# Performance work log

Measured on AMD Instinct MI355X. Metric: run time of the kernel, lower is better.

Reference implementation:

```python
import jax, jax.numpy as jnp
import numpy as np

N_AGENT, N_TRACK, D_IN, HEADS, OUT, E = 50000, 200000, 128, 4, 64, 500000
NEG_SLOPE = 0.2  # PyG GATConv default negative_slope


def segment_softmax(scores, seg, n):
    # PyG softmax: subtract per-segment max, exp, divide by per-segment sum (+1e-16)
    m = jax.ops.segment_max(scores, seg, num_segments=n)
    m = jnp.where(jnp.isneginf(m), 0.0, m)  # guard empty segments
    e = jnp.exp(scores - m[seg])
    s = jax.ops.segment_sum(e, seg, num_segments=n)
    return e / (s[seg] + 1e-16)


def gat_conv(x_src, x_dst, e_src, e_dst, W, a_src, a_dst, b):
    # PyG GATConv, concat=False, add_self_loops=False, eval mode (no dropout)
    H, C = a_src.shape
    n_dst = x_dst.shape[0]
    xs = (x_src @ W).reshape(-1, H, C)   # [Ns,H,C]
    xd = (x_dst @ W).reshape(-1, H, C)   # [Nd,H,C] (same lin for src and dst)
    al_s = jnp.einsum('nhc,hc->nh', xs, a_src)
    al_d = jnp.einsum('nhc,hc->nh', xd, a_dst)
    alpha = jax.nn.leaky_relu(al_s[e_src] + al_d[e_dst], NEG_SLOPE)  # [E,H]
    alpha = segment_softmax(alpha, e_dst, n_dst)
    msg = xs[e_src] * alpha[:, :, None]                               # [E,H,C]
    out = jax.ops.segment_sum(msg, e_dst, num_segments=n_dst)         # [Nd,H,C]
    return out.mean(axis=1) + b  # concat=False -> mean over heads, then bias


def setup_inputs() -> dict:
    key = jax.random.key(0)
    ks = jax.random.split(key, 16)
    inp = {
        'x_agent': jax.random.normal(ks[0], (N_AGENT, D_IN), jnp.float32),
        'x_track': jax.random.normal(ks[1], (N_TRACK, D_IN), jnp.float32),
        'W': jax.random.normal(ks[2], (4, D_IN, HEADS * OUT), jnp.float32) * 0.1,
        'att_src': jax.random.normal(ks[3], (4, HEADS, OUT), jnp.float32) * 0.1,
        'att_dst': jax.random.normal(ks[4], (4, HEADS, OUT), jnp.float32) * 0.1,
        'bias': jax.random.normal(ks[5], (4, OUT), jnp.float32) * 0.1,
    }
    # relations 0,2: agent->track ; relations 1,3: track->agent
    srcs = [N_AGENT, N_TRACK, N_AGENT, N_TRACK]
    dsts = [N_TRACK, N_AGENT, N_TRACK, N_AGENT]
    for r in range(4):
        inp[f'e{r}_src'] = jax.random.randint(ks[6 + 2 * r], (E,), 0, srcs[r], jnp.int32)
        inp[f'e{r}_dst'] = jax.random.randint(ks[7 + 2 * r], (E,), 0, dsts[r], jnp.int32)
    return inp


def reference(x_agent, x_track, W, att_src, att_dst, bias,
              e0_src, e0_dst, e1_src, e1_dst, e2_src, e2_dst, e3_src, e3_dst):
    t0 = gat_conv(x_agent, x_track, e0_src, e0_dst, W[0], att_src[0], att_dst[0], bias[0])
    a1 = gat_conv(x_track, x_agent, e1_src, e1_dst, W[1], att_src[1], att_dst[1], bias[1])
    t2 = gat_conv(x_agent, x_track, e2_src, e2_dst, W[2], att_src[2], att_dst[2], bias[2])
    a3 = gat_conv(x_track, x_agent, e3_src, e3_dst, W[3], att_src[3], att_dst[3], bias[3])
    # HeteroConv aggr='mean' over relations sharing a dst node type
    out_agent = (a1 + a3) * 0.5
    out_track = (t0 + t2) * 0.5
    return out_agent, out_track
```

## Files before the change

### kernel.cpp

```cpp
#include <hip/hip_runtime.h>
#include <hip/hip_bf16.h>

typedef __attribute__((ext_vector_type(8))) short short8;
typedef __attribute__((ext_vector_type(4))) short short4v;
typedef __attribute__((ext_vector_type(4))) float f32x4;

__device__ __forceinline__ unsigned short f2bf(float f) {
  unsigned u = __builtin_bit_cast(unsigned, f);
  u += 0x7FFFu + ((u >> 16) & 1u);
  return (unsigned short)(u >> 16);
}
__device__ __forceinline__ float bf2f(unsigned short b) {
  unsigned u = ((unsigned)b) << 16;
  return __builtin_bit_cast(float, u);
}

__global__ void prep_u(const float* __restrict__ W, const float* __restrict__ att_src,
                       const float* __restrict__ att_dst,
                       float* __restrict__ U_agent, float* __restrict__ U_track) {
  int idx = blockIdx.x * 256 + threadIdx.x;
  if (idx >= 2 * 16 * 128) return;
  int which = idx >> 11;
  int rem = idx & 2047;
  int j = rem >> 7;
  int k = rem & 127;
  int r = j >> 2, h = j & 3;
  bool srcSide = (which == 0) ? ((r & 1) == 0) : ((r & 1) == 1);
  const float* att = (srcSide ? att_src : att_dst) + (r * 4 + h) * 64;
  const float* Wr = W + (r * 128 + k) * 256 + h * 64;
  float s = 0.f;
#pragma unroll 8
  for (int c = 0; c < 64; ++c) s += Wr[c] * att[c];
  (which ? U_track : U_agent)[j * 128 + k] = s;
}

__global__ void prep_wt(const float* __restrict__ W, unsigned short* __restrict__ Wt) {
  int idx = blockIdx.x * 256 + threadIdx.x;
  if (idx >= 4 * 256 * 128) return;
  int r = idx >> 15;
  int rem = idx & 32767;
  int c = rem >> 7;
  int k = rem & 127;
  Wt[idx] = f2bf(W[(r * 128 + k) * 256 + c]);
}

__global__ __launch_bounds__(256) void node_al2(const float* __restrict__ x,
                                                const float* __restrict__ U, int N,
                                                float* __restrict__ d0, float* __restrict__ d1,
                                                float* __restrict__ d2, float* __restrict__ d3) {
  __shared__ float xs[32 * 132];
  __shared__ float us[16 * 132];
  int tid = threadIdx.x;
  for (int i = tid; i < 2048; i += 256) us[(i >> 7) * 132 + (i & 127)] = U[i];
  int n0 = blockIdx.x * 32;
#pragma unroll
  for (int it = 0; it < 4; ++it) {
    int idx = (it * 256 + tid) * 4;
    int row = idx >> 7, k = idx & 127;
    float4 v = make_float4(0.f, 0.f, 0.f, 0.f);
    if (n0 + row < N) v = *(const float4*)(x + (size_t)(n0 + row) * 128 + k);
    *(float4*)&xs[row * 132 + k] = v;
  }
  __syncthreads();
  int node = tid >> 3;
  int g = n0 + node;
  if (g >= N) return;
  int j0 = (tid & 7) * 2;
  const float* xr = &xs[node * 132];
  const float* u0 = &us[j0 * 132];
  const float* u1 = &us[(j0 + 1) * 132];
  float a0 = 0.f, a1 = 0.f;
#pragma unroll
  for (int k = 0; k < 128; k += 4) {
    float4 xv = *(const float4*)(xr + k);
    float4 v0 = *(const float4*)(u0 + k);
    float4 v1 = *(const float4*)(u1 + k);
    a0 += xv.x * v0.x + xv.y * v0.y + xv.z * v0.z + xv.w * v0.w;
    a1 += xv.x * v1.x + xv.y * v1.y + xv.z * v1.z + xv.w * v1.w;
  }
  int r = j0 >> 2, h = j0 & 3;
  float* dp = (r == 0) ? d0 : (r == 1) ? d1 : (r == 2) ? d2 : d3;
  dp[(size_t)g * 4 + h] = a0;
  dp[(size_t)g * 4 + h + 1] = a1;
}

__global__ void init_out(float* __restrict__ out, const float* __restrict__ bias,
                         int NA, int NT) {
  int idx = blockIdx.x * 256 + threadIdx.x;
  int total4 = (NA + NT) * 16;
  if (idx >= total4) return;
  int f = idx * 4;
  int c = f & 63;
  const float *b0, *b1;
  if (f < NA * 64) { b0 = bias + 64; b1 = bias + 192; }
  else             { b0 = bias;      b1 = bias + 128; }
  float4 v;
  v.x = 0.5f * (b0[c] + b1[c]);
  v.y = 0.5f * (b0[c + 1] + b1[c + 1]);
  v.z = 0.5f * (b0[c + 2] + b1[c + 2]);
  v.w = 0.5f * (b0[c + 3] + b1[c + 3]);
  *(float4*)(out + f) = v;
}

__global__ __launch_bounds__(256) void proj_gemm(const float* __restrict__ X,
                                                 const unsigned short* __restrict__ Wt,
                                                 unsigned short* __restrict__ P, int Ns) {
  __shared__ unsigned short Xs[64 * 136];
  __shared__ unsigned short Ws[128 * 136];
  int tid = threadIdx.x;
  int m0 = blockIdx.x * 64;
  int cs = blockIdx.y * 128;
#pragma unroll
  for (int it = 0; it < 8; ++it) {
    int idx = (tid + it * 256) * 4;
    int row = idx >> 7, k = idx & 127;
    int g = m0 + row;
    float4 v = make_float4(0.f, 0.f, 0.f, 0.f);
    if (g < Ns) v = *(const float4*)(X + (size_t)g * 128 + k);
    short4v sv;
    sv.x = (short)f2bf(v.x); sv.y = (short)f2bf(v.y);
    sv.z = (short)f2bf(v.z); sv.w = (short)f2bf(v.w);
    *(short4v*)&Xs[row * 136 + k] = sv;
  }
#pragma unroll
  for (int it = 0; it < 8; ++it) {
    int idx = (tid + it * 256) * 8;
    int row = idx >> 7, k = idx & 127;
    short8 v = *(const short8*)(Wt + (size_t)(cs + row) * 128 + k);
    *(short8*)&Ws[row * 136 + k] = v;
  }
  __syncthreads();
  int lane = tid & 63, w = tid >> 6;
  f32x4 acc[8];
#pragma unroll
  for (int t = 0; t < 8; ++t) acc[t] = (f32x4){0.f, 0.f, 0.f, 0.f};
  int aoff = (w * 16 + (lane & 15)) * 136 + (lane >> 4) * 8;
  int boff = (lane & 15) * 136 + (lane >> 4) * 8;
#pragma unroll
  for (int kc = 0; kc < 4; ++kc) {
    short8 a = *(const short8*)&Xs[aoff + kc * 32];
#pragma unroll
    for (int t = 0; t < 8; ++t) {
      short8 b = *(const short8*)&Ws[boff + t * 16 * 136 + kc * 32];
      acc[t] = __builtin_amdgcn_mfma_f32_16x16x32_bf16(a, b, acc[t], 0, 0, 0);
    }
  }
#pragma unroll
  for (int t = 0; t < 8; ++t) {
#pragma unroll
    for (int q = 0; q < 4; ++q) {
      int grow = m0 + w * 16 + (lane >> 4) * 4 + q;
      if (grow < Ns) P[(size_t)grow * 256 + cs + t * 16 + (lane & 15)] = f2bf(acc[t][q]);
    }
  }
}

__global__ void csr_hist(const int* __restrict__ edst, int* __restrict__ count, int E) {
  int e = blockIdx.x * 256 + threadIdx.x;
  if (e < E) atomicAdd(&count[edst[e]], 1);
}

__global__ void csr_base(const int* __restrict__ count, int* __restrict__ cursor,
                         int* __restrict__ base, int* __restrict__ fill, int Nd) {
  int d = blockIdx.x * 256 + threadIdx.x;
  if (d >= Nd) return;
  int c = count[d];
  int b = atomicAdd(cursor, c);
  base[d] = b;
  fill[d] = b;
}

__global__ void csr_scatter(const int* __restrict__ esrc, const int* __restrict__ edst,
                            int* __restrict__ fill, int* __restrict__ elist, int E) {
  int e = blockIdx.x * 256 + threadIdx.x;
  if (e < E) {
    int pos = atomicAdd(&fill[edst[e]], 1);
    elist[pos] = esrc[e];
  }
}

__global__ __launch_bounds__(256) void passB_v3(
    const int* __restrict__ count, const int* __restrict__ base,
    const int* __restrict__ elist,
    const float* __restrict__ alS, const float* __restrict__ alD,
    const unsigned short* __restrict__ P, float* __restrict__ outp, int Nd) {
  int grp = (blockIdx.x * 256 + threadIdx.x) >> 5;
  if (grp >= Nd) return;
  int l = threadIdx.x & 31;
  int h = l >> 3;
  int cb = (l & 7) * 8;
  int cnt = count[grp];
  int b = base[grp];
  float ad = alD[(size_t)grp * 4 + h];
  int loff = h * 64 + cb;

  float den = 0.f;
  float acc[8];
#pragma unroll
  for (int j = 0; j < 8; ++j) acc[j] = 0.f;

  for (int i = 0; i < cnt; i += 2) {
    bool two = (i + 1 < cnt);
    int s0 = elist[b + i];
    int s1 = two ? elist[b + i + 1] : s0;
    float v0 = alS[(size_t)s0 * 4 + h] + ad;
    float v1 = alS[(size_t)s1 * 4 + h] + ad;
    short8 p0 = *(const short8*)(P + (size_t)s0 * 256 + loff);
    short8 p1 = *(const short8*)(P + (size_t)s1 * 256 + loff);
    v0 = v0 > 0.f ? v0 : 0.2f * v0;
    v1 = v1 > 0.f ? v1 : 0.2f * v1;
    float e0 = __expf(v0);
    float e1 = two ? __expf(v1) : 0.f;
    den += e0 + e1;
#pragma unroll
    for (int j = 0; j < 8; ++j)
      acc[j] += e0 * bf2f((unsigned short)p0[j]) + e1 * bf2f((unsigned short)p1[j]);
  }

  float q = 0.125f / (den + 1e-16f);
#pragma unroll
  for (int j = 0; j < 8; ++j) {
    float a = acc[j] * q;
    a += __shfl_xor(a, 8);
    a += __shfl_xor(a, 16);
    acc[j] = a;
  }
  if (l < 8) {
    float* op = outp + (size_t)grp * 64 + l * 8;
    float4 c0 = *(float4*)op;
    float4 c1 = *(float4*)(op + 4);
    c0.x += acc[0]; c0.y += acc[1]; c0.z += acc[2]; c0.w += acc[3];
    c1.x += acc[4]; c1.y += acc[5]; c1.z += acc[6]; c1.w += acc[7];
    *(float4*)op = c0;
    *(float4*)(op + 4) = c1;
  }
}

extern "C" void kernel_launch(void* const* d_in, const int* in_sizes, int n_in,
                              void* d_out, int out_size, void* d_ws, size_t ws_size,
                              hipStream_t stream) {
  const float* x_agent = (const float*)d_in[0];
  const float* x_track = (const float*)d_in[1];
  const float* W = (const float*)d_in[2];
  const float* att_src = (const float*)d_in[3];
  const float* att_dst = (const float*)d_in[4];
  const float* bias = (const float*)d_in[5];
  const int* es[4] = {(const int*)d_in[6], (const int*)d_in[8],
                      (const int*)d_in[10], (const int*)d_in[12]};
  const int* ed[4] = {(const int*)d_in[7], (const int*)d_in[9],
                      (const int*)d_in[11], (const int*)d_in[13]};
  int NA = in_sizes[0] / 128;
  int NT = in_sizes[1] / 128;
  float* out = (float*)d_out;

  int Ns[4] = {NA, NT, NA, NT};
  int Nd[4] = {NT, NA, NT, NA};
  const float* xsrc[4] = {x_agent, x_track, x_agent, x_track};

  char* ws = (char*)d_ws;
  size_t off = 0;
  auto alloc = [&](size_t bytes) -> void* {
    void* p = ws + off;
    off += (bytes + 255) & ~(size_t)255;
    return p;
  };
  int maxN = NA > NT ? NA : NT;
  int maxE = 0;
  for (int r = 0; r < 4; ++r) maxE = in_sizes[6 + 2 * r] > maxE ? in_sizes[6 + 2 * r] : maxE;

  unsigned short* P = (unsigned short*)alloc((size_t)maxN * 256 * 2);
  float *alS[4], *alD[4];
  for (int r = 0; r < 4; ++r) alS[r] = (float*)alloc((size_t)Ns[r] * 4 * 4);
  for (int r = 0; r < 4; ++r) alD[r] = (float*)alloc((size_t)Nd[r] * 4 * 4);
  float* U_agent = (float*)alloc(16 * 128 * 4);
  float* U_track = (float*)alloc(16 * 128 * 4);
  unsigned short* Wt = (unsigned short*)alloc(4 * 256 * 128 * 2);
  int* count = (int*)alloc(((size_t)maxN + 1) * 4);
  int* base = (int*)alloc((size_t)maxN * 4);
  int* fill = (int*)alloc((size_t)maxN * 4);
  int* elist = (int*)alloc((size_t)maxE * 4);

  prep_u<<<16, 256, 0, stream>>>(W, att_src, att_dst, U_agent, U_track);
  prep_wt<<<512, 256, 0, stream>>>(W, Wt);

  node_al2<<<(NA + 31) / 32, 256, 0, stream>>>(x_agent, U_agent, NA,
                                               alS[0], alD[1], alS[2], alD[3]);
  node_al2<<<(NT + 31) / 32, 256, 0, stream>>>(x_track, U_track, NT,
                                               alD[0], alS[1], alD[2], alS[3]);

  int total4 = (NA + NT) * 16;
  init_out<<<(total4 + 255) / 256, 256, 0, stream>>>(out, bias, NA, NT);

  for (int r = 0; r < 4; ++r) {
    int E = in_sizes[6 + 2 * r];
    int nd = Nd[r];
    int* cursor = count + maxN;
    hipMemsetAsync(count, 0, ((size_t)maxN + 1) * 4, stream);
    csr_hist<<<(E + 255) / 256, 256, 0, stream>>>(ed[r], count, E);
    csr_base<<<(nd + 255) / 256, 256, 0, stream>>>(count, cursor, base, fill, nd);
    csr_scatter<<<(E + 255) / 256, 256, 0, stream>>>(es[r], ed[r], fill, elist, E);

    dim3 pg((Ns[r] + 63) / 64, 2);
    proj_gemm<<<pg, 256, 0, stream>>>(xsrc[r], Wt + (size_t)r * 256 * 128, P, Ns[r]);

    float* outp = (r & 1) ? out : out + (size_t)NA * 64;
    passB_v3<<<(nd + 7) / 8, 256, 0, stream>>>(count, base, elist,
                                               alS[r], alD[r], P, outp, nd);
  }
}
```

Baseline: 971.5 us.

## Fuse agent-to-track relations into one CSR and aggregation pass, drop init_out

Relations 0 and 2 now share one CSR build, with both edge lists stored per destination and source indices offset into a stacked projection buffer. A single passB_track kernel then aggregates both relations per track node and writes the final output with the averaged bias. The separate init_out pass and the read-modify-write of the output are removed for the first write to each output region. This saves launches, one output init pass and one read-modify-write over the track output, at the cost of a larger P buffer and more code.

Measured after the change: 849.4 us. 12.6% less time.

```diff
diff --git a/kernel.cpp b/kernel.cpp
--- a/kernel.cpp
+++ b/kernel.cpp
@@ -34,6 +34,13 @@
   (which ? U_track : U_agent)[j * 128 + k] = s;
 }
 
+__global__ void prep_bias(const float* __restrict__ bias,
+                          float* __restrict__ bavgT, float* __restrict__ bavgA) {
+  int c = threadIdx.x;
+  if (c < 64) bavgT[c] = 0.5f * (bias[c] + bias[128 + c]);
+  else if (c < 128) bavgA[c - 64] = 0.5f * (bias[64 + c - 64] + bias[192 + c - 64]);
+}
+
 __global__ void prep_wt(const float* __restrict__ W, unsigned short* __restrict__ Wt) {
   int idx = blockIdx.x * 256 + threadIdx.x;
   if (idx >= 4 * 256 * 128) return;
@@ -82,24 +89,6 @@
   float* dp = (r == 0) ? d0 : (r == 1) ? d1 : (r == 2) ? d2 : d3;
   dp[(size_t)g * 4 + h] = a0;
   dp[(size_t)g * 4 + h + 1] = a1;
-}
-
-__global__ void init_out(float* __restrict__ out, const float* __restrict__ bias,
-                         int NA, int NT) {
-  int idx = blockIdx.x * 256 + threadIdx.x;
-  int total4 = (NA + NT) * 16;
-  if (idx >= total4) return;
-  int f = idx * 4;
-  int c = f & 63;
-  const float *b0, *b1;
-  if (f < NA * 64) { b0 = bias + 64; b1 = bias + 192; }
-  else             { b0 = bias;      b1 = bias + 128; }
-  float4 v;
-  v.x = 0.5f * (b0[c] + b1[c]);
-  v.y = 0.5f * (b0[c + 1] + b1[c + 1]);
-  v.z = 0.5f * (b0[c + 2] + b1[c + 2]);
-  v.w = 0.5f * (b0[c + 3] + b1[c + 3]);
-  *(float4*)(out + f) = v;
 }
 
 __global__ __launch_bounds__(256) void proj_gemm(const float* __restrict__ X,
@@ -160,45 +149,140 @@
   if (e < E) atomicAdd(&count[edst[e]], 1);
 }
 
-__global__ void csr_base(const int* __restrict__ count, int* __restrict__ cursor,
-                         int* __restrict__ base, int* __restrict__ fill, int Nd) {
+__global__ void csr_base2(const int* __restrict__ cntA, const int* __restrict__ cntB,
+                          int* __restrict__ cursor, int* __restrict__ base,
+                          int* __restrict__ fillA, int* __restrict__ fillB, int Nd) {
   int d = blockIdx.x * 256 + threadIdx.x;
   if (d >= Nd) return;
-  int c = count[d];
-  int b = atomicAdd(cursor, c);
+  int c0 = cntA[d], c2 = cntB[d];
+  int b = atomicAdd(cursor, c0 + c2);
   base[d] = b;
-  fill[d] = b;
+  fillA[d] = b;
+  fillB[d] = b + c0;
 }
 
 __global__ void csr_scatter(const int* __restrict__ esrc, const int* __restrict__ edst,
-                            int* __restrict__ fill, int* __restrict__ elist, int E) {
+                            int* __restrict__ fill, int* __restrict__ elist,
+                            int rowoff, int E) {
   int e = blockIdx.x * 256 + threadIdx.x;
   if (e < E) {
     int pos = atomicAdd(&fill[edst[e]], 1);
-    elist[pos] = esrc[e];
-  }
-}
-
-__global__ __launch_bounds__(256) void passB_v3(
-    const int* __restrict__ count, const int* __restrict__ base,
-    const int* __restrict__ elist,
-    const float* __restrict__ alS, const float* __restrict__ alD,
-    const unsigned short* __restrict__ P, float* __restrict__ outp, int Nd) {
+    elist[pos] = esrc[e] + rowoff;
+  }
+}
+
+__global__ __launch_bounds__(256) void passB_track(
+    const int* __restrict__ cntA, const int* __restrict__ cntB,
+    const int* __restrict__ base, const int* __restrict__ elist,
+    const float* __restrict__ alSA, const float* __restrict__ alD0,
+    const float* __restrict__ alD2, const unsigned short* __restrict__ P,
+    const float* __restrict__ bavg, float* __restrict__ outp, int Nd) {
   int grp = (blockIdx.x * 256 + threadIdx.x) >> 5;
   if (grp >= Nd) return;
   int l = threadIdx.x & 31;
   int h = l >> 3;
-  int cb = (l & 7) * 8;
+  int loff = h * 64 + (l & 7) * 8;
+  int c0 = cntA[grp], c2 = cntB[grp];
+  int b = base[grp];
+  float ad0 = alD0[(size_t)grp * 4 + h];
+  float ad2 = alD2[(size_t)grp * 4 + h];
+
+  float res[8];
+#pragma unroll
+  for (int j = 0; j < 8; ++j) res[j] = 0.f;
+  float acc[8];
+
+  {
+    float den = 0.f;
+#pragma unroll
+    for (int j = 0; j < 8; ++j) acc[j] = 0.f;
+    for (int i = 0; i < c0; i += 2) {
+      bool two = (i + 1 < c0);
+      int s0 = elist[b + i];
+      int s1 = two ? elist[b + i + 1] : s0;
+      float v0 = alSA[(size_t)s0 * 4 + h] + ad0;
+      float v1 = alSA[(size_t)s1 * 4 + h] + ad0;
+      short8 p0 = *(const short8*)(P + (size_t)s0 * 256 + loff);
+      short8 p1 = *(const short8*)(P + (size_t)s1 * 256 + loff);
+      v0 = v0 > 0.f ? v0 : 0.2f * v0;
+      v1 = v1 > 0.f ? v1 : 0.2f * v1;
+      float e0 = __expf(v0);
+      float e1 = two ? __expf(v1) : 0.f;
+      den += e0 + e1;
+#pragma unroll
+      for (int j = 0; j < 8; ++j)
+        acc[j] += e0 * bf2f((unsigned short)p0[j]) + e1 * bf2f((unsigned short)p1[j]);
+    }
+    float q = 0.125f / (den + 1e-16f);
+#pragma unroll
+    for (int j = 0; j < 8; ++j) res[j] += acc[j] * q;
+  }
+  {
+    float den = 0.f;
+#pragma unroll
+    for (int j = 0; j < 8; ++j) acc[j] = 0.f;
+    int bb = b + c0;
+    for (int i = 0; i < c2; i += 2) {
+      bool two = (i + 1 < c2);
+      int s0 = elist[bb + i];
+      int s1 = two ? elist[bb + i + 1] : s0;
+      float v0 = alSA[(size_t)s0 * 4 + h] + ad2;
+      float v1 = alSA[(size_t)s1 * 4 + h] + ad2;
+      short8 p0 = *(const short8*)(P + (size_t)s0 * 256 + loff);
+      short8 p1 = *(const short8*)(P + (size_t)s1 * 256 + loff);
+      v0 = v0 > 0.f ? v0 : 0.2f * v0;
+      v1 = v1 > 0.f ? v1 : 0.2f * v1;
+      float e0 = __expf(v0);
+      float e1 = two ? __expf(v1) : 0.f;
+      den += e0 + e1;
+#pragma unroll
+      for (int j = 0; j < 8; ++j)
+        acc[j] += e0 * bf2f((unsigned short)p0[j]) + e1 * bf2f((unsigned short)p1[j]);
+    }
+    float q = 0.125f / (den + 1e-16f);
+#pragma unroll
+    for (int j = 0; j < 8; ++j) res[j] += acc[j] * q;
+  }
+
+#pragma unroll
+  for (int j = 0; j < 8; ++j) {
+    float a = res[j];
+    a += __shfl_xor(a, 8);
+    a += __shfl_xor(a, 16);
+    res[j] = a;
+  }
+  if (l < 8) {
+    float* op = outp + (size_t)grp * 64 + l * 8;
+    const float* bv = bavg + l * 8;
+    float4 c0v, c1v;
+    c0v.x = bv[0] + res[0]; c0v.y = bv[1] + res[1];
+    c0v.z = bv[2] + res[2]; c0v.w = bv[3] + res[3];
+    c1v.x = bv[4] + res[4]; c1v.y = bv[5] + res[5];
+    c1v.z = bv[6] + res[6]; c1v.w = bv[7] + res[7];
+    *(float4*)op = c0v;
+    *(float4*)(op + 4) = c1v;
+  }
+}
+
+__global__ __launch_bounds__(256) void passB_one(
+    const int* __restrict__ count, const int* __restrict__ base,
+    const int* __restrict__ elist,
+    const float* __restrict__ alS, const float* __restrict__ alD,
+    const unsigned short* __restrict__ P, const float* __restrict__ bavg,
+    float* __restrict__ outp, int Nd, int mode) {
+  int grp = (blockIdx.x * 256 + threadIdx.x) >> 5;
+  if (grp >= Nd) return;
+  int l = threadIdx.x & 31;
+  int h = l >> 3;
+  int loff = h * 64 + (l & 7) * 8;
   int cnt = count[grp];
   int b = base[grp];
   float ad = alD[(size_t)grp * 4 + h];
-  int loff = h * 64 + cb;
 
   float den = 0.f;
   float acc[8];
 #pragma unroll
   for (int j = 0; j < 8; ++j) acc[j] = 0.f;
-
   for (int i = 0; i < cnt; i += 2) {
     bool two = (i + 1 < cnt);
     int s0 = elist[b + i];
@@ -216,7 +300,6 @@
     for (int j = 0; j < 8; ++j)
       acc[j] += e0 * bf2f((unsigned short)p0[j]) + e1 * bf2f((unsigned short)p1[j]);
   }
-
   float q = 0.125f / (den + 1e-16f);
 #pragma unroll
   for (int j = 0; j < 8; ++j) {
@@ -227,12 +310,23 @@
   }
   if (l < 8) {
     float* op = outp + (size_t)grp * 64 + l * 8;
-    float4 c0 = *(float4*)op;
-    float4 c1 = *(float4*)(op + 4);
-    c0.x += acc[0]; c0.y += acc[1]; c0.z += acc[2]; c0.w += acc[3];
-    c1.x += acc[4]; c1.y += acc[5]; c1.z += acc[6]; c1.w += acc[7];
-    *(float4*)op = c0;
-    *(float4*)(op + 4) = c1;
+    if (mode == 0) {
+      const float* bv = bavg + l * 8;
+      float4 c0v, c1v;
+      c0v.x = bv[0] + acc[0]; c0v.y = bv[1] + acc[1];
+      c0v.z = bv[2] + acc[2]; c0v.w = bv[3] + acc[3];
+      c1v.x = bv[4] + acc[4]; c1v.y = bv[5] + acc[5];
+      c1v.z = bv[6] + acc[6]; c1v.w = bv[7] + acc[7];
+      *(float4*)op = c0v;
+      *(float4*)(op + 4) = c1v;
+    } else {
+      float4 c0v = *(float4*)op;
+      float4 c1v = *(float4*)(op + 4);
+      c0v.x += acc[0]; c0v.y += acc[1]; c0v.z += acc[2]; c0v.w += acc[3];
+      c1v.x += acc[4]; c1v.y += acc[5]; c1v.z += acc[6]; c1v.w += acc[7];
+      *(float4*)op = c0v;
+      *(float4*)(op + 4) = c1v;
+    }
   }
 }
 
@@ -251,11 +345,10 @@
                       (const int*)d_in[11], (const int*)d_in[13]};
   int NA = in_sizes[0] / 128;
   int NT = in_sizes[1] / 128;
+  int E0 = in_sizes[6], E1 = in_sizes[8], E2 = in_sizes[10], E3 = in_sizes[12];
   float* out = (float*)d_out;
-
-  int Ns[4] = {NA, NT, NA, NT};
-  int Nd[4] = {NT, NA, NT, NA};
-  const float* xsrc[4] = {x_agent, x_track, x_agent, x_track};
+  float* out_agent = out;
+  float* out_track = out + (size_t)NA * 64;
 
   char* ws = (char*)d_ws;
   size_t off = 0;
@@ -265,46 +358,73 @@
     return p;
   };
   int maxN = NA > NT ? NA : NT;
-  int maxE = 0;
-  for (int r = 0; r < 4; ++r) maxE = in_sizes[6 + 2 * r] > maxE ? in_sizes[6 + 2 * r] : maxE;
-
-  unsigned short* P = (unsigned short*)alloc((size_t)maxN * 256 * 2);
-  float *alS[4], *alD[4];
-  for (int r = 0; r < 4; ++r) alS[r] = (float*)alloc((size_t)Ns[r] * 4 * 4);
-  for (int r = 0; r < 4; ++r) alD[r] = (float*)alloc((size_t)Nd[r] * 4 * 4);
+  int prow_max = (2 * NA > NT) ? 2 * NA : NT;
+  int elist_max = E0 + E2;
+  if (E1 > elist_max) elist_max = E1;
+  if (E3 > elist_max) elist_max = E3;
+
+  unsigned short* P = (unsigned short*)alloc((size_t)prow_max * 256 * 2);
+  float* alSA = (float*)alloc((size_t)2 * NA * 4 * 4);
+  float* alST = (float*)alloc((size_t)2 * NT * 4 * 4);
+  float* alD0 = (float*)alloc((size_t)NT * 4 * 4);
+  float* alD1 = (float*)alloc((size_t)NA * 4 * 4);
+  float* alD2 = (float*)alloc((size_t)NT * 4 * 4);
+  float* alD3 = (float*)alloc((size_t)NA * 4 * 4);
   float* U_agent = (float*)alloc(16 * 128 * 4);
   float* U_track = (float*)alloc(16 * 128 * 4);
+  float* bavgT = (float*)alloc(64 * 4);
+  float* bavgA = (float*)alloc(64 * 4);
   unsigned short* Wt = (unsigned short*)alloc(4 * 256 * 128 * 2);
-  int* count = (int*)alloc(((size_t)maxN + 1) * 4);
+  int* ints0 = (int*)alloc(((size_t)2 * maxN + 64) * 4);
+  int* cntA = ints0;
+  int* cntB = ints0 + maxN;
+  int* cursor = ints0 + 2 * maxN;
   int* base = (int*)alloc((size_t)maxN * 4);
-  int* fill = (int*)alloc((size_t)maxN * 4);
-  int* elist = (int*)alloc((size_t)maxE * 4);
+  int* fillA = (int*)alloc((size_t)maxN * 4);
+  int* fillB = (int*)alloc((size_t)maxN * 4);
+  int* elist = (int*)alloc((size_t)elist_max * 4);
 
   prep_u<<<16, 256, 0, stream>>>(W, att_src, att_dst, U_agent, U_track);
+  prep_bias<<<1, 128, 0, stream>>>(bias, bavgT, bavgA);
   prep_wt<<<512, 256, 0, stream>>>(W, Wt);
 
   node_al2<<<(NA + 31) / 32, 256, 0, stream>>>(x_agent, U_agent, NA,
-                                               alS[0], alD[1], alS[2], alD[3]);
+                                               alSA, alD1, alSA + (size_t)NA * 4, alD3);
   node_al2<<<(NT + 31) / 32, 256, 0, stream>>>(x_track, U_track, NT,
-                                               alD[0], alS[1], alD[2], alS[3]);
-
-  int total4 = (NA + NT) * 16;
-  init_out<<<(total4 + 255) / 256, 256, 0, stream>>>(out, bias, NA, NT);
-
-  for (int r = 0; r < 4; ++r) {
-    int E = in_sizes[6 + 2 * r];
-    int nd = Nd[r];
-    int* cursor = count + maxN;
-    hipMemsetAsync(count, 0, ((size_t)maxN + 1) * 4, stream);
-    csr_hist<<<(E + 255) / 256, 256, 0, stream>>>(ed[r], count, E);
-    csr_base<<<(nd + 255) / 256, 256, 0, stream>>>(count, cursor, base, fill, nd);
-    csr_scatter<<<(E + 255) / 256, 256, 0, stream>>>(es[r], ed[r], fill, elist, E);
-
-    dim3 pg((Ns[r] + 63) / 64, 2);
-    proj_gemm<<<pg, 256, 0, stream>>>(xsrc[r], Wt + (size_t)r * 256 * 128, P, Ns[r]);
-
-    float* outp = (r & 1) ? out : out + (size_t)NA * 64;
-    passB_v3<<<(nd + 7) / 8, 256, 0, stream>>>(count, base, elist,
-                                               alS[r], alD[r], P, outp, nd);
-  }
-}
+                                               alD0, alST, alD2, alST + (size_t)NT * 4);
+
+  hipMemsetAsync(ints0, 0, ((size_t)2 * maxN + 64) * 4, stream);
+  csr_hist<<<(E0 + 255) / 256, 256, 0, stream>>>(ed[0], cntA, E0);
+  csr_hist<<<(E2 + 255) / 256, 256, 0, stream>>>(ed[2], cntB, E2);
+  csr_base2<<<(NT + 255) / 256, 256, 0, stream>>>(cntA, cntB, cursor, base, fillA, fillB, NT);
+  csr_scatter<<<(E0 + 255) / 256, 256, 0, stream>>>(es[0], ed[0], fillA, elist, 0, E0);
+  csr_scatter<<<(E2 + 255) / 256, 256, 0, stream>>>(es[2], ed[2], fillB, elist, NA, E2);
+
+  dim3 pgA((NA + 63) / 64, 2);
+  proj_gemm<<<pgA, 256, 0, stream>>>(x_agent, Wt + 0 * 256 * 128, P, NA);
+  proj_gemm<<<pgA, 256, 0, stream>>>(x_agent, Wt + (size_t)2 * 256 * 128,
+                                     P + (size_t)NA * 256, NA);
+
+  passB_track<<<(NT + 7) / 8, 256, 0, stream>>>(cntA, cntB, base, elist,
+                                                alSA, alD0, alD2, P, bavgT,
+                                                out_track, NT);
+
+  dim3 pgT((NT + 63) / 64, 2);
+
+  hipMemsetAsync(ints0, 0, ((size_t)2 * maxN + 64) * 4, stream);
+  csr_hist<<<(E1 + 255) / 256, 256, 0, stream>>>(ed[1], cntA, E1);
+  csr_base2<<<(NA + 255) / 256, 256, 0, stream>>>(cntA, cntB, cursor, base, fillA, fillB, NA);
+  csr_scatter<<<(E1 + 255) / 256, 256, 0, stream>>>(es[1], ed[1], fillA, elist, 0, E1);
+  proj_gemm<<<pgT, 256, 0, stream>>>(x_track, Wt + (size_t)1 * 256 * 128, P, NT);
+  passB_one<<<(NA + 7) / 8, 256, 0, stream>>>(cntA, base, elist, alST, alD1, P,
+                                              bavgA, out_agent, NA, 0);
+
+  hipMemsetAsync(ints0, 0, ((size_t)2 * maxN + 64) * 4, stream);
+  csr_hist<<<(E3 + 255) / 256, 256, 0, stream>>>(ed[3], cntA, E3);
+  csr_base2<<<(NA + 255) / 256, 256, 0, stream>>>(cntA, cntB, cursor, base, fillA, fillB, NA);
+  csr_scatter<<<(E3 + 255) / 256, 256, 0, stream>>>(es[3], ed[3], fillA, elist, 0, E3);
+  proj_gemm<<<pgT, 256, 0, stream>>>(x_track, Wt + (size_t)3 * 256 * 128, P, NT);
+  passB_one<<<(NA + 7) / 8, 256, 0, stream>>>(cntA, base, elist,
+                                              alST + (size_t)NT * 4, alD3, P,
+                                              bavgA, out_agent, NA, 1);
+}
```
